# Kernel tuning notes

Hardware: AMD Instinct MI355X
Metric: run time of the kernel (lower is better)

Reference implementation:

```python
import jax, jax.numpy as jnp
import numpy as np

K = 10          # neighbors, hard-coded in MLP1.forward
NEG_SLOPE = 0.2 # LeakyReLU slope
EPS = 1e-5      # BatchNorm2d default eps


def setup_inputs() -> dict:
    key = jax.random.key(0)
    k1, k2, k3, k4 = jax.random.split(key, 4)
    B, C, N = 8, 6, 4096
    x = jax.random.normal(k1, (B, C, N), dtype=jnp.float32)
    W = jax.random.normal(k2, (64, 6), dtype=jnp.float32) * 0.2      # conv1x1 weight (O, I)
    gamma = jax.random.uniform(k3, (64,), jnp.float32, 0.5, 1.5)     # BN weight
    beta = jax.random.normal(k4, (64,), dtype=jnp.float32) * 0.1     # BN bias
    return {"x": x, "W": W, "gamma": gamma, "beta": beta}


def _knn_idx(x3, k):
    # pairwise_distance[b,i,j] = -||x_i - x_j||^2 (as in the torch knn)
    inner = jnp.einsum('bdn,bdm->bnm', x3, x3)          # x_i . x_j
    xx = jnp.sum(x3 * x3, axis=1)                       # (B, N)
    pd = 2.0 * inner - xx[:, :, None] - xx[:, None, :]  # (B, N, N)
    _, idx = jax.lax.top_k(pd, k)                       # k nearest (incl. self)
    return idx                                          # (B, N, k) int32


def reference(x, W, gamma, beta):
    # x: (B, 6, N)
    idx = _knn_idx(x[:, :3], K)                          # (B, N, k)
    # gather neighbor features: feat[b,c,n,j] = x[b,c,idx[b,n,j]]
    feat = jax.vmap(lambda xb, ib: xb[:, ib])(x, idx)    # (B, 6, N, k)
    # center xyz over the k neighbors and scale by 10
    xyz = feat[:, :3]
    xyz = (xyz - jnp.mean(xyz, axis=-1, keepdims=True)) * 10.0
    feat = jnp.concatenate([xyz, feat[:, 3:]], axis=1)   # (B, 6, N, k)
    # 1x1 conv (6 -> 64), no bias
    y = jnp.einsum('oc,bcnk->bonk', W, feat)             # (B, 64, N, k)
    # BatchNorm2d in train mode: batch stats over (B, N, k), biased variance
    mu = jnp.mean(y, axis=(0, 2, 3), keepdims=True)
    var = jnp.mean((y - mu) ** 2, axis=(0, 2, 3), keepdims=True)
    y = (y - mu) * jax.lax.rsqrt(var + EPS)
    y = y * gamma[None, :, None, None] + beta[None, :, None, None]
    # LeakyReLU(0.2)
    y = jnp.where(y >= 0, y, NEG_SLOPE * y)
    # max over neighbors k
    y = jnp.max(y, axis=-1)                              # (B, 64, N)
    # global max + mean pooling over N, concat along last axis
    x1 = jnp.max(y, axis=-1)                             # (B, 64)
    x2 = jnp.mean(y, axis=-1)                            # (B, 64)
    return jnp.concatenate([x1, x2], axis=-1)            # (B, 128)
```

## Files before the change

### kernel.cpp

```cpp
#include <hip/hip_runtime.h>
#include <float.h>

#define K_NN 10
#define BATCH 8
#define CIN 6
#define NPTS 4096
#define COUT 64
#define NSEG 8
#define SEGLEN (NPTS / NSEG)
#define CHUNK 16
#define NCHUNK (SEGLEN / CHUNK)
#define NWORD (SEGLEN / 32)
#define NEG_SLOPE 0.2f
#define BN_EPS 1e-5f

static constexpr size_t OFF_IDX = 0;
static constexpr size_t OFF_PTS = OFF_IDX + (size_t)BATCH * K_NN * NPTS * sizeof(int);
static constexpr size_t OFF_Q   = OFF_PTS + (size_t)BATCH * NPTS * sizeof(float4);
static constexpr size_t SZ_Q    = (size_t)NSEG * BATCH * NPTS * K_NN * sizeof(int);
static constexpr size_t OFF_ST  = OFF_Q + SZ_Q;

__device__ __forceinline__ float wave_sum(float v) {
#pragma unroll
    for (int m = 32; m >= 1; m >>= 1) v += __shfl_xor(v, m, 64);
    return v;
}
__device__ __forceinline__ float wave_max(float v) {
#pragma unroll
    for (int m = 32; m >= 1; m >>= 1) v = fmaxf(v, __shfl_xor(v, m, 64));
    return v;
}

__device__ __forceinline__ float distp(float qx, float qy, float qz, float4 c) {
    return fmaf(c.x, qx, fmaf(c.y, qy, fmaf(c.z, qz, -c.w)));
}

__device__ __forceinline__ float fmax3(float a, float b, float c) {
    return fmaxf(fmaxf(a, b), c);
}

#define CHL(cj) { float _hi = fmaxf(cj, t); t = fminf(cj, t); cj = _hi; }

#define CSWP(va, vb, ia, ib) \
    if (va > vb) { float _tv = va; va = vb; vb = _tv; int _ti = ia; ia = ib; ib = _ti; }

#define INSERT10(dd, mm) \
    if ((dd) > v9) { \
        v9 = (dd); i9 = (mm); \
        CSWP(v9, v8, i9, i8) \
        CSWP(v8, v7, i8, i7) \
        CSWP(v7, v6, i7, i6) \
        CSWP(v6, v5, i6, i5) \
        CSWP(v5, v4, i5, i4) \
        CSWP(v4, v3, i4, i3) \
        CSWP(v3, v2, i3, i2) \
        CSWP(v2, v1, i2, i1) \
        CSWP(v1, v0, i1, i0) \
    }

__global__ __launch_bounds__(256) void prep_pts(const float* __restrict__ x,
                                                float4* __restrict__ pts,
                                                double* __restrict__ stats) {
    if (blockIdx.x == 0 && threadIdx.x < 27) stats[threadIdx.x] = 0.0;
    int t = blockIdx.x * 256 + threadIdx.x;
    int b = t >> 12;
    int n = t & (NPTS - 1);
    const float* xb = x + (size_t)b * CIN * NPTS;
    float x0 = xb[n];
    float x1 = xb[NPTS + n];
    float x2 = xb[2 * NPTS + n];
    pts[t] = make_float4(2.0f * x0, 2.0f * x1, 2.0f * x2, x0 * x0 + x1 * x1 + x2 * x2);
}

__global__ __launch_bounds__(256, 4) void knn_part(const float4* __restrict__ pts,
                                                   int* __restrict__ part) {
    int b = blockIdx.y;
    int s = blockIdx.z;
    int n = blockIdx.x * 256 + threadIdx.x;
    const float4* p = pts + (size_t)b * NPTS;
    float4 q4 = p[n];
    float qx = 0.5f * q4.x, qy = 0.5f * q4.y, qz = 0.5f * q4.z;
    int m0 = s * SEGLEN;

    float c0 = -FLT_MAX, c1 = -FLT_MAX, c2 = -FLT_MAX, c3 = -FLT_MAX, c4 = -FLT_MAX;
    float c5 = -FLT_MAX, c6 = -FLT_MAX, c7 = -FLT_MAX, c8 = -FLT_MAX, c9 = -FLT_MAX;

    for (int ch = 0; ch < NCHUNK; ch++) {
        const float4* cp = p + (m0 + ch * CHUNK);
        float d0  = distp(qx, qy, qz, cp[0]);
        float d1  = distp(qx, qy, qz, cp[1]);
        float d2  = distp(qx, qy, qz, cp[2]);
        float d3  = distp(qx, qy, qz, cp[3]);
        float d4  = distp(qx, qy, qz, cp[4]);
        float d5  = distp(qx, qy, qz, cp[5]);
        float d6  = distp(qx, qy, qz, cp[6]);
        float d7  = distp(qx, qy, qz, cp[7]);
        float d8  = distp(qx, qy, qz, cp[8]);
        float d9  = distp(qx, qy, qz, cp[9]);
        float d10 = distp(qx, qy, qz, cp[10]);
        float d11 = distp(qx, qy, qz, cp[11]);
        float d12 = distp(qx, qy, qz, cp[12]);
        float d13 = distp(qx, qy, qz, cp[13]);
        float d14 = distp(qx, qy, qz, cp[14]);
        float d15 = distp(qx, qy, qz, cp[15]);
        float a0 = fmax3(d0, d1, d2);
        float a1 = fmax3(d3, d4, d5);
        float a2 = fmax3(d6, d7, d8);
        float a3 = fmax3(d9, d10, d11);
        float a4 = fmax3(d12, d13, d14);
        float t = fmaxf(fmax3(fmax3(a0, a1, a2), a3, a4), d15);
        CHL(c0) CHL(c1) CHL(c2) CHL(c3) CHL(c4)
        CHL(c5) CHL(c6) CHL(c7) CHL(c8) CHL(c9)
    }
    float thr = c9;

    float v0 = -FLT_MAX, v1 = -FLT_MAX, v2 = -FLT_MAX, v3 = -FLT_MAX, v4 = -FLT_MAX;
    float v5 = -FLT_MAX, v6 = -FLT_MAX, v7 = -FLT_MAX, v8 = -FLT_MAX, v9 = -FLT_MAX;
    int i0 = 0, i1 = 0, i2 = 0, i3 = 0, i4 = 0;
    int i5 = 0, i6 = 0, i7 = 0, i8 = 0, i9 = 0;

    for (int w = 0; w < NWORD; w++) {
        const float4* cp = p + (m0 + w * 32);
        unsigned int mask = 0u;
#pragma unroll
        for (int u = 0; u < 32; u++) {
            float d = distp(qx, qy, qz, cp[u]);
            mask = (mask << 1) | (d >= thr ? 1u : 0u);
        }
        int base = m0 + w * 32;
        while (mask) {
            int j = __builtin_clz(mask);
            mask ^= (0x80000000u >> j);
            int m = base + j;
            float4 cc = p[m];
            float d = distp(qx, qy, qz, cc);
            INSERT10(d, m)
        }
    }

    int* o = part + (((size_t)s * BATCH + b) * K_NN) * NPTS + n;
    o[(size_t)0 * NPTS] = i0;
    o[(size_t)1 * NPTS] = i1;
    o[(size_t)2 * NPTS] = i2;
    o[(size_t)3 * NPTS] = i3;
    o[(size_t)4 * NPTS] = i4;
    o[(size_t)5 * NPTS] = i5;
    o[(size_t)6 * NPTS] = i6;
    o[(size_t)7 * NPTS] = i7;
    o[(size_t)8 * NPTS] = i8;
    o[(size_t)9 * NPTS] = i9;
}

__global__ __launch_bounds__(256, 8) void merge_kernel(const float4* __restrict__ pts,
                                                       const int* __restrict__ part,
                                                       int* __restrict__ idxo) {
    __shared__ float dml[4][K_NN][64];
    __shared__ unsigned short iml[4][K_NN][64];

    int b  = blockIdx.y;
    int ln = threadIdx.x & 63;
    int wv = threadIdx.x >> 6;
    int wvu = __builtin_amdgcn_readfirstlane(wv);
    int n  = blockIdx.x * 64 + ln;
    const float4* p = pts + (size_t)b * NPTS;
    float4 q4 = p[n];
    float qx = 0.5f * q4.x, qy = 0.5f * q4.y, qz = 0.5f * q4.z;

    float v0 = -FLT_MAX, v1 = -FLT_MAX, v2 = -FLT_MAX, v3 = -FLT_MAX, v4 = -FLT_MAX;
    float v5 = -FLT_MAX, v6 = -FLT_MAX, v7 = -FLT_MAX, v8 = -FLT_MAX, v9 = -FLT_MAX;
    int i0 = 0, i1 = 0, i2 = 0, i3 = 0, i4 = 0;
    int i5 = 0, i6 = 0, i7 = 0, i8 = 0, i9 = 0;

#pragma unroll
    for (int t = 0; t < 2; t++) {
        int s = 2 * wvu + t;
        const int* pp = part + (((size_t)s * BATCH + b) * K_NN) * NPTS + n;
#pragma unroll
        for (int j = 0; j < K_NN; j++) {
            int m = pp[(size_t)j * NPTS];
            float4 cc = p[m];
            float d = distp(qx, qy, qz, cc);
            INSERT10(d, m)
        }
    }

    dml[wv][0][ln] = v0; iml[wv][0][ln] = (unsigned short)i0;
    dml[wv][1][ln] = v1; iml[wv][1][ln] = (unsigned short)i1;
    dml[wv][2][ln] = v2; iml[wv][2][ln] = (unsigned short)i2;
    dml[wv][3][ln] = v3; iml[wv][3][ln] = (unsigned short)i3;
    dml[wv][4][ln] = v4; iml[wv][4][ln] = (unsigned short)i4;
    dml[wv][5][ln] = v5; iml[wv][5][ln] = (unsigned short)i5;
    dml[wv][6][ln] = v6; iml[wv][6][ln] = (unsigned short)i6;
    dml[wv][7][ln] = v7; iml[wv][7][ln] = (unsigned short)i7;
    dml[wv][8][ln] = v8; iml[wv][8][ln] = (unsigned short)i8;
    dml[wv][9][ln] = v9; iml[wv][9][ln] = (unsigned short)i9;
    __syncthreads();

    if (wvu == 0) {
        float v0 = -FLT_MAX, v1 = -FLT_MAX, v2 = -FLT_MAX, v3 = -FLT_MAX, v4 = -FLT_MAX;
        float v5 = -FLT_MAX, v6 = -FLT_MAX, v7 = -FLT_MAX, v8 = -FLT_MAX, v9 = -FLT_MAX;
        int i0 = 0, i1 = 0, i2 = 0, i3 = 0, i4 = 0;
        int i5 = 0, i6 = 0, i7 = 0, i8 = 0, i9 = 0;
#pragma unroll
        for (int w = 0; w < 4; w++) {
#pragma unroll
            for (int j = 0; j < K_NN; j++) {
                float d = dml[w][j][ln];
                int m = iml[w][j][ln];
                INSERT10(d, m)
            }
        }
        int* o = idxo + (size_t)b * K_NN * NPTS + n;
        o[(size_t)0 * NPTS] = i0;
        o[(size_t)1 * NPTS] = i1;
        o[(size_t)2 * NPTS] = i2;
        o[(size_t)3 * NPTS] = i3;
        o[(size_t)4 * NPTS] = i4;
        o[(size_t)5 * NPTS] = i5;
        o[(size_t)6 * NPTS] = i6;
        o[(size_t)7 * NPTS] = i7;
        o[(size_t)8 * NPTS] = i8;
        o[(size_t)9 * NPTS] = i9;
    }
}

__global__ __launch_bounds__(256) void feat_kernel(const float4* __restrict__ pts,
                                                   const float* __restrict__ x,
                                                   const float* __restrict__ W,
                                                   const int* __restrict__ idx,
                                                   float* __restrict__ q,
                                                   double* __restrict__ stats) {
    __shared__ float sW[COUT * CIN];
    __shared__ float sred[4][27];
    for (int i = threadIdx.x; i < COUT * CIN; i += 256) sW[i] = W[i];
    __syncthreads();

    int b = blockIdx.y;
    int og = blockIdx.z;
    int n = blockIdx.x * 256 + threadIdx.x;
    const float* xb = x + (size_t)b * CIN * NPTS;
    const float4* p = pts + (size_t)b * NPTS;

    int nb[K_NN];
#pragma unroll
    for (int k = 0; k < K_NN; k++) nb[k] = idx[((size_t)b * K_NN + k) * NPTS + n];

    float f[CIN][K_NN];
#pragma unroll
    for (int k = 0; k < K_NN; k++) {
        float4 c = p[nb[k]];
        f[0][k] = 0.5f * c.x; f[1][k] = 0.5f * c.y; f[2][k] = 0.5f * c.z;
    }
#pragma unroll
    for (int c = 3; c < CIN; c++)
#pragma unroll
        for (int k = 0; k < K_NN; k++)
            f[c][k] = xb[c * NPTS + nb[k]];

#pragma unroll
    for (int c = 0; c < 3; c++) {
        float s = 0.f;
#pragma unroll
        for (int k = 0; k < K_NN; k++) s += f[c][k];
        float m = s / 10.0f;
#pragma unroll
        for (int k = 0; k < K_NN; k++) f[c][k] = (f[c][k] - m) * 10.0f;
    }

    float* qb = q + (size_t)b * COUT * NPTS + n;
    int o0 = og * 16;
#pragma unroll
    for (int oo = 0; oo < 16; oo++) {
        int o = o0 + oo;
        float w0 = sW[o * 6 + 0], w1 = sW[o * 6 + 1], w2 = sW[o * 6 + 2];
        float w3 = sW[o * 6 + 3], w4 = sW[o * 6 + 4], w5 = sW[o * 6 + 5];
        float mx = -FLT_MAX;
#pragma unroll
        for (int k = 0; k < K_NN; k++) {
            float y = w0 * f[0][k] + w1 * f[1][k] + w2 * f[2][k] +
                      w3 * f[3][k] + w4 * f[4][k] + w5 * f[5][k];
            mx = fmaxf(mx, y);
        }
        qb[(size_t)o * NPTS] = mx;
    }

    if (og != 0) return;

    float s1[CIN];
#pragma unroll
    for (int c = 0; c < CIN; c++) {
        float s = 0.f;
#pragma unroll
        for (int k = 0; k < K_NN; k++) s += f[c][k];
        s1[c] = s;
    }
    float s2[21];
#pragma unroll
    for (int i = 0; i < 21; i++) s2[i] = 0.f;
#pragma unroll
    for (int k = 0; k < K_NN; k++) {
        int pp = 0;
#pragma unroll
        for (int c = 0; c < CIN; c++)
#pragma unroll
            for (int c2 = c; c2 < CIN; c2++) {
                s2[pp] += f[c][k] * f[c2][k];
                pp++;
            }
    }
#pragma unroll
    for (int c = 0; c < CIN; c++) s1[c] = wave_sum(s1[c]);
#pragma unroll
    for (int i = 0; i < 21; i++) s2[i] = wave_sum(s2[i]);

    int wv = threadIdx.x >> 6;
    int ln = threadIdx.x & 63;
    if (ln == 0) {
#pragma unroll
        for (int c = 0; c < CIN; c++) sred[wv][c] = s1[c];
#pragma unroll
        for (int i = 0; i < 21; i++) sred[wv][6 + i] = s2[i];
    }
    __syncthreads();
    if (threadIdx.x < 27) {
        float t = sred[0][threadIdx.x] + sred[1][threadIdx.x] +
                  sred[2][threadIdx.x] + sred[3][threadIdx.x];
        atomicAdd(&stats[threadIdx.x], (double)t);
    }
}

__global__ __launch_bounds__(256) void reduce_kernel(const float* __restrict__ q,
                                                     const double* __restrict__ stats,
                                                     const float* __restrict__ W,
                                                     const float* __restrict__ gamma,
                                                     const float* __restrict__ beta,
                                                     float* __restrict__ out) {
    int o = blockIdx.x;
    int b = blockIdx.y;

    __shared__ float s_sc, s_sh;
    if (threadIdx.x == 0) {
        const double minv = 1.0 / (double)((size_t)BATCH * NPTS * K_NN);
        double w[CIN];
#pragma unroll
        for (int c = 0; c < CIN; c++) w[c] = (double)W[o * CIN + c];
        double mu = 0.0;
#pragma unroll
        for (int c = 0; c < CIN; c++) mu += w[c] * stats[c];
        mu *= minv;
        double ey2 = 0.0;
        int pp = 6;
#pragma unroll
        for (int c = 0; c < CIN; c++)
#pragma unroll
            for (int c2 = c; c2 < CIN; c2++) {
                double v = w[c] * w[c2] * stats[pp];
                ey2 += (c2 == c) ? v : 2.0 * v;
                pp++;
            }
        ey2 *= minv;
        double var = ey2 - mu * mu;
        float scale = gamma[o] * rsqrtf((float)var + BN_EPS);
        float shift = beta[o] - (float)mu * scale;
        s_sc = scale;
        s_sh = shift;
    }
    __syncthreads();
    float scale = s_sc, shift = s_sh;

    const float* qp = q + ((size_t)b * COUT + o) * NPTS;
    float mx = -FLT_MAX, sm = 0.f;
    for (int i = threadIdx.x; i < NPTS; i += 256) {
        float z = scale * qp[i] + shift;
        z = (z >= 0.f) ? z : NEG_SLOPE * z;
        mx = fmaxf(mx, z);
        sm += z;
    }
    mx = wave_max(mx);
    sm = wave_sum(sm);
    __shared__ float smx[4], ssm2[4];
    int wv = threadIdx.x >> 6;
    int ln = threadIdx.x & 63;
    if (ln == 0) { smx[wv] = mx; ssm2[wv] = sm; }
    __syncthreads();
    if (threadIdx.x == 0) {
        float m = fmaxf(fmaxf(smx[0], smx[1]), fmaxf(smx[2], smx[3]));
        float s = ssm2[0] + ssm2[1] + ssm2[2] + ssm2[3];
        out[b * 2 * COUT + o] = m;
        out[b * 2 * COUT + COUT + o] = s * (1.0f / (float)NPTS);
    }
}

extern "C" void kernel_launch(void* const* d_in, const int* in_sizes, int n_in,
                              void* d_out, int out_size, void* d_ws, size_t ws_size,
                              hipStream_t stream) {
    const float* x     = (const float*)d_in[0];
    const float* W     = (const float*)d_in[1];
    const float* gamma = (const float*)d_in[2];
    const float* beta  = (const float*)d_in[3];
    float* out = (float*)d_out;

    char* ws = (char*)d_ws;
    int*    idx   = (int*)(ws + OFF_IDX);
    float4* pts   = (float4*)(ws + OFF_PTS);
    int*    part  = (int*)(ws + OFF_Q);
    float*  q     = (float*)(ws + OFF_Q);
    double* stats = (double*)(ws + OFF_ST);

    prep_pts<<<BATCH * NPTS / 256, 256, 0, stream>>>(x, pts, stats);
    knn_part<<<dim3(NPTS / 256, BATCH, NSEG), 256, 0, stream>>>(pts, part);
    merge_kernel<<<dim3(NPTS / 64, BATCH), 256, 0, stream>>>(pts, part, idx);
    feat_kernel<<<dim3(NPTS / 256, BATCH, 4), 256, 0, stream>>>(pts, x, W, idx, q, stats);
    reduce_kernel<<<dim3(COUT, BATCH), 256, 0, stream>>>(q, stats, W, gamma, beta, out);
}
```

Baseline: 180.2 us.

## Use packed dual-point distances and candidate lists instead of per-segment top-10 insert

```diff
diff --git a/kernel.cpp b/kernel.cpp
--- a/kernel.cpp
+++ b/kernel.cpp
@@ -8,17 +8,20 @@
 #define COUT 64
 #define NSEG 8
 #define SEGLEN (NPTS / NSEG)
-#define CHUNK 16
+#define CHUNK 8
 #define NCHUNK (SEGLEN / CHUNK)
-#define NWORD (SEGLEN / 32)
+#define CAP 20
 #define NEG_SLOPE 0.2f
 #define BN_EPS 1e-5f
 
-static constexpr size_t OFF_IDX = 0;
-static constexpr size_t OFF_PTS = OFF_IDX + (size_t)BATCH * K_NN * NPTS * sizeof(int);
-static constexpr size_t OFF_Q   = OFF_PTS + (size_t)BATCH * NPTS * sizeof(float4);
-static constexpr size_t SZ_Q    = (size_t)NSEG * BATCH * NPTS * K_NN * sizeof(int);
-static constexpr size_t OFF_ST  = OFF_Q + SZ_Q;
+static constexpr size_t OFF_IDX  = 0;
+static constexpr size_t OFF_PTS  = OFF_IDX + (size_t)BATCH * K_NN * NPTS * sizeof(int);
+static constexpr size_t OFF_PTSP = OFF_PTS + (size_t)BATCH * NPTS * sizeof(float4);
+static constexpr size_t OFF_Q    = OFF_PTSP + (size_t)BATCH * NPTS * sizeof(float4);
+static constexpr size_t SZ_Q     = (size_t)NSEG * BATCH * NPTS * CAP * sizeof(unsigned short);
+static constexpr size_t OFF_ST   = OFF_Q + SZ_Q;
+
+typedef float v2f __attribute__((ext_vector_type(2)));
 
 __device__ __forceinline__ float wave_sum(float v) {
 #pragma unroll
@@ -33,6 +36,21 @@
 
 __device__ __forceinline__ float distp(float qx, float qy, float qz, float4 c) {
     return fmaf(c.x, qx, fmaf(c.y, qy, fmaf(c.z, qz, -c.w)));
+}
+
+__device__ __forceinline__ v2f dist2(v2f qx2, v2f qy2, v2f qz2, float4 fa, float4 fb) {
+    v2f cx = {fa.x, fa.y}, cy = {fa.z, fa.w}, cz = {fb.x, fb.y}, cw = {fb.z, fb.w};
+#if __has_builtin(__builtin_elementwise_fma)
+    v2f t = __builtin_elementwise_fma(cz, qz2, -cw);
+    t = __builtin_elementwise_fma(cy, qy2, t);
+    t = __builtin_elementwise_fma(cx, qx2, t);
+    return t;
+#else
+    v2f t;
+    t[0] = fmaf(cx[0], qx2[0], fmaf(cy[0], qy2[0], fmaf(cz[0], qz2[0], -cw[0])));
+    t[1] = fmaf(cx[1], qx2[1], fmaf(cy[1], qy2[1], fmaf(cz[1], qz2[1], -cw[1])));
+    return t;
+#endif
 }
 
 __device__ __forceinline__ float fmax3(float a, float b, float c) {
@@ -60,99 +78,96 @@
 
 __global__ __launch_bounds__(256) void prep_pts(const float* __restrict__ x,
                                                 float4* __restrict__ pts,
+                                                float4* __restrict__ ptsp,
                                                 double* __restrict__ stats) {
     if (blockIdx.x == 0 && threadIdx.x < 27) stats[threadIdx.x] = 0.0;
     int t = blockIdx.x * 256 + threadIdx.x;
     int b = t >> 12;
     int n = t & (NPTS - 1);
     const float* xb = x + (size_t)b * CIN * NPTS;
-    float x0 = xb[n];
-    float x1 = xb[NPTS + n];
-    float x2 = xb[2 * NPTS + n];
-    pts[t] = make_float4(2.0f * x0, 2.0f * x1, 2.0f * x2, x0 * x0 + x1 * x1 + x2 * x2);
+    float X = xb[n];
+    float Y = xb[NPTS + n];
+    float Z = xb[2 * NPTS + n];
+    float w = X * X + Y * Y + Z * Z;
+    pts[t] = make_float4(2.0f * X, 2.0f * Y, 2.0f * Z, w);
+    float Xn = __shfl_down(X, 1, 64);
+    float Yn = __shfl_down(Y, 1, 64);
+    float Zn = __shfl_down(Z, 1, 64);
+    float wn = __shfl_down(w, 1, 64);
+    if ((n & 1) == 0) {
+        float4* pb = ptsp + (size_t)b * NPTS;
+        pb[n]     = make_float4(2.0f * X, 2.0f * Xn, 2.0f * Y, 2.0f * Yn);
+        pb[n + 1] = make_float4(2.0f * Z, 2.0f * Zn, w, wn);
+    }
 }
 
 __global__ __launch_bounds__(256, 4) void knn_part(const float4* __restrict__ pts,
-                                                   int* __restrict__ part) {
+                                                   const float4* __restrict__ ptsp,
+                                                   unsigned short* __restrict__ part) {
     int b = blockIdx.y;
     int s = blockIdx.z;
     int n = blockIdx.x * 256 + threadIdx.x;
-    const float4* p = pts + (size_t)b * NPTS;
+    const float4* p  = pts  + (size_t)b * NPTS;
+    const float4* p2 = ptsp + (size_t)b * NPTS;
     float4 q4 = p[n];
     float qx = 0.5f * q4.x, qy = 0.5f * q4.y, qz = 0.5f * q4.z;
+    v2f qx2 = {qx, qx}, qy2 = {qy, qy}, qz2 = {qz, qz};
     int m0 = s * SEGLEN;
 
     float c0 = -FLT_MAX, c1 = -FLT_MAX, c2 = -FLT_MAX, c3 = -FLT_MAX, c4 = -FLT_MAX;
     float c5 = -FLT_MAX, c6 = -FLT_MAX, c7 = -FLT_MAX, c8 = -FLT_MAX, c9 = -FLT_MAX;
 
     for (int ch = 0; ch < NCHUNK; ch++) {
-        const float4* cp = p + (m0 + ch * CHUNK);
-        float d0  = distp(qx, qy, qz, cp[0]);
-        float d1  = distp(qx, qy, qz, cp[1]);
-        float d2  = distp(qx, qy, qz, cp[2]);
-        float d3  = distp(qx, qy, qz, cp[3]);
-        float d4  = distp(qx, qy, qz, cp[4]);
-        float d5  = distp(qx, qy, qz, cp[5]);
-        float d6  = distp(qx, qy, qz, cp[6]);
-        float d7  = distp(qx, qy, qz, cp[7]);
-        float d8  = distp(qx, qy, qz, cp[8]);
-        float d9  = distp(qx, qy, qz, cp[9]);
-        float d10 = distp(qx, qy, qz, cp[10]);
-        float d11 = distp(qx, qy, qz, cp[11]);
-        float d12 = distp(qx, qy, qz, cp[12]);
-        float d13 = distp(qx, qy, qz, cp[13]);
-        float d14 = distp(qx, qy, qz, cp[14]);
-        float d15 = distp(qx, qy, qz, cp[15]);
-        float a0 = fmax3(d0, d1, d2);
-        float a1 = fmax3(d3, d4, d5);
-        float a2 = fmax3(d6, d7, d8);
-        float a3 = fmax3(d9, d10, d11);
-        float a4 = fmax3(d12, d13, d14);
-        float t = fmaxf(fmax3(fmax3(a0, a1, a2), a3, a4), d15);
+        const float4* cp = p2 + (m0 + ch * CHUNK);
+        v2f e0 = dist2(qx2, qy2, qz2, cp[0], cp[1]);
+        v2f e1 = dist2(qx2, qy2, qz2, cp[2], cp[3]);
+        v2f e2 = dist2(qx2, qy2, qz2, cp[4], cp[5]);
+        v2f e3 = dist2(qx2, qy2, qz2, cp[6], cp[7]);
+        float a0 = fmax3(e0[0], e0[1], e1[0]);
+        float a1 = fmax3(e1[1], e2[0], e2[1]);
+        float a2 = fmax3(e3[0], e3[1], a0);
+        float t = fmaxf(a1, a2);
         CHL(c0) CHL(c1) CHL(c2) CHL(c3) CHL(c4)
         CHL(c5) CHL(c6) CHL(c7) CHL(c8) CHL(c9)
     }
     float thr = c9;
 
-    float v0 = -FLT_MAX, v1 = -FLT_MAX, v2 = -FLT_MAX, v3 = -FLT_MAX, v4 = -FLT_MAX;
-    float v5 = -FLT_MAX, v6 = -FLT_MAX, v7 = -FLT_MAX, v8 = -FLT_MAX, v9 = -FLT_MAX;
-    int i0 = 0, i1 = 0, i2 = 0, i3 = 0, i4 = 0;
-    int i5 = 0, i6 = 0, i7 = 0, i8 = 0, i9 = 0;
-
-    for (int w = 0; w < NWORD; w++) {
-        const float4* cp = p + (m0 + w * 32);
-        unsigned int mask = 0u;
-#pragma unroll
-        for (int u = 0; u < 32; u++) {
-            float d = distp(qx, qy, qz, cp[u]);
-            mask = (mask << 1) | (d >= thr ? 1u : 0u);
-        }
-        int base = m0 + w * 32;
-        while (mask) {
-            int j = __builtin_clz(mask);
-            mask ^= (0x80000000u >> j);
-            int m = base + j;
-            float4 cc = p[m];
-            float d = distp(qx, qy, qz, cc);
+    unsigned short* o = part + (((size_t)s * BATCH + b) * CAP) * NPTS + n;
+    int cnt = 0;
+    for (int pr = 0; pr < SEGLEN / 2; pr++) {
+        v2f d2 = dist2(qx2, qy2, qz2, p2[m0 + 2 * pr], p2[m0 + 2 * pr + 1]);
+        int m = m0 + 2 * pr;
+        if (d2[0] >= thr) { o[(size_t)min(cnt, CAP - 1) * NPTS] = (unsigned short)m;       cnt++; }
+        if (d2[1] >= thr) { o[(size_t)min(cnt, CAP - 1) * NPTS] = (unsigned short)(m + 1); cnt++; }
+    }
+    for (int j = cnt; j < CAP; j++) o[(size_t)j * NPTS] = 0xFFFFu;
+
+    if (cnt > CAP) {
+        float v0 = -FLT_MAX, v1 = -FLT_MAX, v2 = -FLT_MAX, v3 = -FLT_MAX, v4 = -FLT_MAX;
+        float v5 = -FLT_MAX, v6 = -FLT_MAX, v7 = -FLT_MAX, v8 = -FLT_MAX, v9 = -FLT_MAX;
+        int i0 = 0, i1 = 0, i2 = 0, i3 = 0, i4 = 0;
+        int i5 = 0, i6 = 0, i7 = 0, i8 = 0, i9 = 0;
+        for (int mm = 0; mm < SEGLEN; mm++) {
+            int m = m0 + mm;
+            float d = distp(qx, qy, qz, p[m]);
             INSERT10(d, m)
         }
-    }
-
-    int* o = part + (((size_t)s * BATCH + b) * K_NN) * NPTS + n;
-    o[(size_t)0 * NPTS] = i0;
-    o[(size_t)1 * NPTS] = i1;
-    o[(size_t)2 * NPTS] = i2;
-    o[(size_t)3 * NPTS] = i3;
-    o[(size_t)4 * NPTS] = i4;
-    o[(size_t)5 * NPTS] = i5;
-    o[(size_t)6 * NPTS] = i6;
-    o[(size_t)7 * NPTS] = i7;
-    o[(size_t)8 * NPTS] = i8;
-    o[(size_t)9 * NPTS] = i9;
+        o[(size_t)0 * NPTS] = (unsigned short)i0;
+        o[(size_t)1 * NPTS] = (unsigned short)i1;
+        o[(size_t)2 * NPTS] = (unsigned short)i2;
+        o[(size_t)3 * NPTS] = (unsigned short)i3;
+        o[(size_t)4 * NPTS] = (unsigned short)i4;
+        o[(size_t)5 * NPTS] = (unsigned short)i5;
+        o[(size_t)6 * NPTS] = (unsigned short)i6;
+        o[(size_t)7 * NPTS] = (unsigned short)i7;
+        o[(size_t)8 * NPTS] = (unsigned short)i8;
+        o[(size_t)9 * NPTS] = (unsigned short)i9;
+        for (int j = K_NN; j < CAP; j++) o[(size_t)j * NPTS] = 0xFFFFu;
+    }
 }
 
 __global__ __launch_bounds__(256, 8) void merge_kernel(const float4* __restrict__ pts,
-                                                       const int* __restrict__ part,
+                                                       const unsigned short* __restrict__ part,
                                                        int* __restrict__ idxo) {
     __shared__ float dml[4][K_NN][64];
     __shared__ unsigned short iml[4][K_NN][64];
@@ -174,10 +189,11 @@
 #pragma unroll
     for (int t = 0; t < 2; t++) {
         int s = 2 * wvu + t;
-        const int* pp = part + (((size_t)s * BATCH + b) * K_NN) * NPTS + n;
-#pragma unroll
-        for (int j = 0; j < K_NN; j++) {
+        const unsigned short* pp = part + (((size_t)s * BATCH + b) * CAP) * NPTS + n;
+#pragma unroll 4
+        for (int j = 0; j < CAP; j++) {
             int m = pp[(size_t)j * NPTS];
+            if (m == 0xFFFF) continue;
             float4 cc = p[m];
             float d = distp(qx, qy, qz, cc);
             INSERT10(d, m)
@@ -403,12 +419,13 @@
     char* ws = (char*)d_ws;
     int*    idx   = (int*)(ws + OFF_IDX);
     float4* pts   = (float4*)(ws + OFF_PTS);
-    int*    part  = (int*)(ws + OFF_Q);
+    float4* ptsp  = (float4*)(ws + OFF_PTSP);
+    unsigned short* part = (unsigned short*)(ws + OFF_Q);
     float*  q     = (float*)(ws + OFF_Q);
     double* stats = (double*)(ws + OFF_ST);
 
-    prep_pts<<<BATCH * NPTS / 256, 256, 0, stream>>>(x, pts, stats);
-    knn_part<<<dim3(NPTS / 256, BATCH, NSEG), 256, 0, stream>>>(pts, part);
+    prep_pts<<<BATCH * NPTS / 256, 256, 0, stream>>>(x, pts, ptsp, stats);
+    knn_part<<<dim3(NPTS / 256, BATCH, NSEG), 256, 0, stream>>>(pts, ptsp, part);
     merge_kernel<<<dim3(NPTS / 64, BATCH), 256, 0, stream>>>(pts, part, idx);
     feat_kernel<<<dim3(NPTS / 256, BATCH, 4), 256, 0, stream>>>(pts, x, W, idx, q, stats);
     reduce_kernel<<<dim3(COUT, BATCH), 256, 0, stream>>>(q, stats, W, gamma, beta, out);
```

Result: slower. 194.1 us (+7.7%).
